# Kernel optimization log

Measured on AMD Instinct MI355X. Metric: run time of the kernel, lower is better.

## Reference

```python
import jax, jax.numpy as jnp
import numpy as np

B, N, C, H, R = 8, 1024, 768, 12, 64
HD = C // H


def setup_inputs() -> dict:
    key = jax.random.key(0)
    ks = jax.random.split(key, 16)
    def nrm(k, shape, s=0.02):
        return jax.random.normal(k, shape, jnp.float32) * s
    return {
        'x': jax.random.normal(ks[0], (B, N, C), jnp.float32),
        'Wqkv': nrm(ks[1], (3 * C, C)),
        'ssf_scale1': 1.0 + nrm(ks[2], (3 * C,)),
        'ssf_shift1': nrm(ks[3], (3 * C,)),
        'Wa': nrm(ks[4], (R, C)),            # LoRA down (sliced to sample_LoRA_dim)
        'Wb': nrm(ks[5], (3 * C, R)),        # LoRA up
        'Wrouter': nrm(ks[6], (2 * H * 3, C)),
        'brouter': nrm(ks[7], (2 * H * 3,)),
        'Wad_down': nrm(ks[8], (R, C)),      # parallel adapter down
        'bad_down': nrm(ks[9], (R,)),
        'Wad_up': nrm(ks[10], (3 * C, R)),   # parallel adapter up -> 3*dim
        'bad_up': nrm(ks[11], (3 * C,)),
        'Wproj': nrm(ks[12], (C, C)),
        'bproj': nrm(ks[13], (C,)),
        'ssf_scale2': 1.0 + nrm(ks[14], (C,)),
        'ssf_shift2': nrm(ks[15], (C,)),
    }


def reference(x, Wqkv, ssf_scale1, ssf_shift1, Wa, Wb, Wrouter, brouter,
              Wad_down, bad_down, Wad_up, bad_up, Wproj, bproj,
              ssf_scale2, ssf_shift2):
    Bx, Nx, Cx = x.shape
    scale = (Cx // H) ** -0.5

    def split_qkv(t):
        t = t.reshape(Bx, Nx, 3, H, Cx // H).transpose(2, 0, 3, 1, 4)
        return t[0], t[1], t[2]

    # base QKV with SSF scale-shift
    q, k, v = split_qkv((x @ Wqkv.T) * ssf_scale1 + ssf_shift1)
    # LoRA delta (dropout inactive at eval)
    ql, kl, vl = split_qkv((x @ Wa.T) @ Wb.T)
    # parallel adapter delta
    qp, kp, vp = split_qkv(jax.nn.gelu(x @ Wad_down.T + bad_down, approximate=False) @ Wad_up.T + bad_up)
    # router gating: sigmoid logits -> [B,N,3,H,2]
    rs = jax.nn.sigmoid(x @ Wrouter.T + brouter).reshape(Bx, Nx, 3, H, 2)
    # faithful to source: raw reshape [B,N,3,H] -> [B,N,H,3] (index-mixing), then transpose(1,2)
    rl = rs[..., 0].reshape(Bx, Nx, H, 3).transpose(0, 2, 1, 3)  # [B,H,N,3]
    rp = rs[..., 1].reshape(Bx, Nx, H, 3).transpose(0, 2, 1, 3)
    q = q + ql * rl[..., 0:1]
    k = k + kl * rl[..., 1:2] + kp * rp[..., 1:2]
    v = v + vl * rl[..., 2:3] + vp * rp[..., 2:3]
    # standard attention (prefix path disabled: prefix_dim=0)
    attn = jax.nn.softmax(jnp.einsum('bhnd,bhmd->bhnm', q, k) * scale, axis=-1)
    o = jnp.einsum('bhnm,bhmd->bhnd', attn, v).transpose(0, 2, 1, 3).reshape(Bx, Nx, Cx)
    return (o @ Wproj.T + bproj) * ssf_scale2 + ssf_shift2
```

## Files before the change

kernel.cpp:

```cpp
#include <hip/hip_runtime.h>
#include <math.h>

typedef unsigned short u16;
typedef unsigned int u32;
typedef short s16x8 __attribute__((ext_vector_type(8)));
typedef float f32x4 __attribute__((ext_vector_type(4)));
typedef float f32x16 __attribute__((ext_vector_type(16)));
typedef u16 u16x4 __attribute__((ext_vector_type(4)));

#define DEVI __device__ __forceinline__

DEVI u16 f2bf(float f) {
  unsigned u = __builtin_bit_cast(unsigned, f);
  u += 0x7fffu + ((u >> 16) & 1u);
  return (u16)(u >> 16);
}

DEVI u32 pack2bf(float a, float b) {
  return (u32)f2bf(a) | ((u32)f2bf(b) << 16);
}

DEVI f32x4 zero4() { f32x4 z; z[0]=0.f; z[1]=0.f; z[2]=0.f; z[3]=0.f; return z; }

DEVI float xor32_max(float x) { return fmaxf(x, __shfl_xor(x, 32, 64)); }
DEVI float xor32_sum(float x) { return x + __shfl_xor(x, 32, 64); }

#define MFMA16(a,b,c) __builtin_amdgcn_mfma_f32_16x16x32_bf16((a),(b),(c),0,0,0)
#define MFMA32(a,b,c) __builtin_amdgcn_mfma_f32_32x32x16_bf16((a),(b),(c),0,0,0)

#define GLD16(gp, lp) __builtin_amdgcn_global_load_lds( \
  (const __attribute__((address_space(1))) void*)(const void*)(gp), \
  (__attribute__((address_space(3))) void*)(void*)(lp), 16, 0, 0)


__global__ __launch_bounds__(256) void prep_x(const float* __restrict__ x,
                                              u16* __restrict__ Aaug) {
  const int i = blockIdx.x * 256 + threadIdx.x;
  if (i >= 8192 * 192) return;
  const int row = i / 192, c4 = (i - row * 192) * 4;
  const float4 v = *(const float4*)(x + (size_t)row * 768 + c4);
  u16x4 o; o[0]=f2bf(v.x); o[1]=f2bf(v.y); o[2]=f2bf(v.z); o[3]=f2bf(v.w);
  *(u16x4*)(Aaug + (size_t)row * 896 + c4) = o;
}

__global__ __launch_bounds__(256) void prep_w(
    const float* __restrict__ Wqkv, const float* __restrict__ s1,
    const float* __restrict__ Wb, const float* __restrict__ Wup,
    const float* __restrict__ Wa, const float* __restrict__ Wdn,
    const float* __restrict__ Wr, const float* __restrict__ Wp,
    u16* __restrict__ Baug, u16* __restrict__ Wsm, u16* __restrict__ Wpj) {
  const int i = blockIdx.x * 256 + threadIdx.x;
  const int N1 = 2304 * 896, N2 = N1 + 256 * 768, N3 = N2 + 768 * 768;
  if (i < N1) {
    const int c = i / 896, kk = i - c * 896;
    float v;
    if (kk < 768)      v = Wqkv[(size_t)c * 768 + kk] * s1[c];
    else if (kk < 832) v = Wb[(size_t)c * 64 + (kk - 768)];
    else               v = Wup[(size_t)c * 64 + (kk - 832)];
    Baug[i] = f2bf(v);
  } else if (i < N2) {
    const int j = i - N1; const int r = j / 768, kk = j - r * 768;
    float v = 0.0f;
    if (r < 64)       v = Wa[(size_t)r * 768 + kk];
    else if (r < 128) v = Wdn[(size_t)(r - 64) * 768 + kk];
    else if (r < 200) v = Wr[(size_t)(r - 128) * 768 + kk];
    Wsm[j] = f2bf(v);
  } else if (i < N3) {
    const int j = i - N2;
    Wpj[j] = f2bf(Wp[j]);
  }
}


template <int MODE>
__global__ __launch_bounds__(256)
void gemm_mfma(const u16* __restrict__ A, int lda,
               const u16* __restrict__ Bt, int ldb,
               const float* __restrict__ p0, const float* __restrict__ p1,
               const float* __restrict__ p2,
               u16* __restrict__ ob0, u16* __restrict__ ob1, u16* __restrict__ ob2,
               float* __restrict__ of0,
               const float* __restrict__ gates) {
  __shared__ __align__(16) u16 lds[2][8192];
  __shared__ float glds[2][2][128];
  const int tid = threadIdx.x;
  const int w = tid >> 6, l = tid & 63;
  const int rl = l & 15, gq = l >> 4;
  const int wrow = (w >> 1) * 64, wcol = (w & 1) * 64;
  const int br = blockIdx.x, bc = blockIdx.y;
  const int nt = (MODE == 2) ? 28 : 24;

  const int srow = l >> 2;
  const int sslot = (l & 3) ^ ((srow >> 1) & 3);
  const u16* aSrc = A + (size_t)(br * 128 + w * 32 + srow) * lda + sslot * 8;
  const u16* bSrc = Bt + (size_t)(bc * 128 + w * 32 + srow) * ldb + sslot * 8;

  int tq = 0;
  if constexpr (MODE == 2) {
    const int g = bc * 2 + (w & 1);
    tq = g / 12;
    {
      const int gsel = tid >> 7, rr = tid & 127;
      const int gg = bc * 2 + gsel;
      const int tt = gg / 12, hh = gg % 12;
      const int f = hh * 3 + tt;
      const int ridx = (f / 12) * 24 + (f % 12) * 2;
      glds[gsel][0][rr] = gates[(size_t)(br * 128 + rr) * 72 + ridx];
      glds[gsel][1][rr] = gates[(size_t)(br * 128 + rr) * 72 + ridx + 1];
    }
  }

  f32x4 acc[4][4];
#pragma unroll
  for (int i = 0; i < 4; ++i)
#pragma unroll
    for (int j = 0; j < 4; ++j) acc[i][j] = zero4();

  auto kt_of = [&](int t) {
    if constexpr (MODE == 2) return (t < 2) ? 26 + t : ((t < 4) ? 22 + t : t - 4);
    else return t;
  };
  auto stage = [&](int kt, int buf) {
    const size_t k0 = (size_t)kt * 32;
    GLD16(aSrc + k0, &lds[buf][(w * 32) * 32]);
    GLD16(aSrc + k0 + (size_t)16 * lda, &lds[buf][(w * 32 + 16) * 32]);
    GLD16(bSrc + k0, &lds[buf][4096 + (w * 32) * 32]);
    GLD16(bSrc + k0 + (size_t)16 * ldb, &lds[buf][4096 + (w * 32 + 16) * 32]);
  };

  stage(kt_of(0), 0);
  __syncthreads();

  for (int t = 0; t < nt; ++t) {
    const int buf = t & 1;
    if (t + 1 < nt) stage(kt_of(t + 1), buf ^ 1);
    const int sl = gq ^ ((rl >> 1) & 3);
    s16x8 af[4], bfv[4];
#pragma unroll
    for (int fr = 0; fr < 4; ++fr) {
      const int row = wrow + fr * 16 + rl;
      af[fr] = *(const s16x8*)&lds[buf][row * 32 + sl * 8];
    }
#pragma unroll
    for (int fc = 0; fc < 4; ++fc) {
      const int row = wcol + fc * 16 + rl;
      bfv[fc] = *(const s16x8*)&lds[buf][4096 + row * 32 + sl * 8];
    }
#pragma unroll
    for (int fr = 0; fr < 4; ++fr)
#pragma unroll
      for (int fc = 0; fc < 4; ++fc)
        acc[fr][fc] = MFMA16(af[fr], bfv[fc], acc[fr][fc]);

    if constexpr (MODE == 2) {
      if (t == 1 || t == 3) {
        const int wsel = w & 1;
        const bool ad = (t == 1);
#pragma unroll
        for (int fr = 0; fr < 4; ++fr)
#pragma unroll
          for (int r = 0; r < 4; ++r) {
            const int rloc = wrow + fr * 16 + gq * 4 + r;
            const float gl = glds[wsel][0][rloc];
            float s;
            if (ad) { const float gp = glds[wsel][1][rloc]; s = (tq > 0) ? gp / gl : 0.0f; }
            else s = gl;
#pragma unroll
            for (int fc = 0; fc < 4; ++fc) acc[fr][fc][r] *= s;
          }
      }
    }
    __syncthreads();
  }

  if constexpr (MODE == 0) {
#pragma unroll
    for (int fc = 0; fc < 4; ++fc) {
      const int col = bc * 128 + wcol + fc * 16 + rl;
#pragma unroll
      for (int fr = 0; fr < 4; ++fr)
#pragma unroll
        for (int r = 0; r < 4; ++r) {
          const int grow = br * 128 + wrow + fr * 16 + gq * 4 + r;
          const float v = acc[fr][fc][r];
          if (col < 64) {
            ob0[(size_t)grow * 896 + 768 + col] = f2bf(v);
          } else if (col < 128) {
            const float u = v + p0[col - 64];
            const float gv = 0.5f * u * (1.0f + erff(u * 0.70710678118654752f));
            ob0[(size_t)grow * 896 + 832 + (col - 64)] = f2bf(gv);
          } else if (col < 200) {
            const float z = v + p1[col - 128];
            of0[(size_t)grow * 72 + (col - 128)] = 1.0f / (1.0f + expf(-z));
          }
        }
    }
  } else if constexpr (MODE == 1) {
#pragma unroll
    for (int fc = 0; fc < 4; ++fc) {
      const int col = bc * 128 + wcol + fc * 16 + rl;
      const float bb = p0[col], sc = p1[col], sf = p2[col];
#pragma unroll
      for (int fr = 0; fr < 4; ++fr)
#pragma unroll
        for (int r = 0; r < 4; ++r) {
          const int grow = br * 128 + wrow + fr * 16 + gq * 4 + r;
          of0[(size_t)grow * 768 + col] = (acc[fr][fc][r] + bb) * sc + sf;
        }
    }
  } else {
    const int wsel = w & 1;
    const int bq = br >> 3;
    const int n0 = (br & 7) * 128;
    const int cbase = bc * 128 + wcol;
    const int hh = (cbase % 768) / 64;
    float s1v[4], buv[4];
#pragma unroll
    for (int fc = 0; fc < 4; ++fc) {
      const int col = cbase + fc * 16 + rl;
      s1v[fc] = p0[col];
      buv[fc] = (tq > 0) ? p1[col] : 0.0f;
    }
    if (tq < 2) {
      u16* dst = (tq == 0) ? ob0 : ob1;
      const float osc = (tq == 0) ? 0.125f : 1.0f;
#pragma unroll
      for (int fr = 0; fr < 4; ++fr)
#pragma unroll
        for (int r = 0; r < 4; ++r) {
          const int rloc = wrow + fr * 16 + gq * 4 + r;
          const float gp = glds[wsel][1][rloc];
          const int n = n0 + rloc;
#pragma unroll
          for (int fc = 0; fc < 4; ++fc) {
            const int d = fc * 16 + rl;
            const float v = (acc[fr][fc][r] + s1v[fc] + gp * buv[fc]) * osc;
            dst[((size_t)(bq * 12 + hh) * 1024 + n) * 64 + d] = f2bf(v);
          }
        }
    } else {
      u16* L = (u16*)&lds[0][0] + (size_t)w * 4096;
#pragma unroll
      for (int fr = 0; fr < 4; ++fr)
#pragma unroll
        for (int r = 0; r < 4; ++r) {
          const int rloc = wrow + fr * 16 + gq * 4 + r;
          const float gp = glds[wsel][1][rloc];
          const int nloc = fr * 16 + gq * 4 + r;
#pragma unroll
          for (int fc = 0; fc < 4; ++fc) {
            const int d = fc * 16 + rl;
            const float v = acc[fr][fc][r] + s1v[fc] + gp * buv[fc];
            L[(d * 64 + nloc) ^ ((d & 7) << 3)] = f2bf(v);
          }
        }
      const int nw = n0 + wrow;
#pragma unroll
      for (int it = 0; it < 8; ++it) {
        const int d = it * 8 + (l >> 3);
        const int slot = l & 7;
        const s16x8 val = *(const s16x8*)&L[d * 64 + ((slot ^ (d & 7)) << 3)];
        *(s16x8*)(ob2 + ((size_t)(bq * 12 + hh) * 64 + d) * 1024 + nw + slot * 8) = val;
      }
    }
  }
}


__global__ __launch_bounds__(256)
void attn2_kernel(const u16* __restrict__ Q, const u16* __restrict__ K,
                  const u16* __restrict__ VT, u16* __restrict__ AO) {
  __shared__ __align__(16) u16 kv[2][8192];
  const int tid = threadIdx.x, w = tid >> 6, l = tid & 63;
  const int l31 = l & 31, hi = l >> 5;
  const int bh = blockIdx.x % 96, qt = blockIdx.x / 96;
  const size_t kb = (size_t)bh * (1024 * 64);
  const float LOG2E = 1.4426950408889634f;
  const float THR = 5.545177f;

  const int q0 = qt * 128 + w * 32;
  s16x8 qf[4];
  {
    const u16* qp = Q + kb + (size_t)(q0 + l31) * 64 + hi * 8;
#pragma unroll
    for (int ks = 0; ks < 4; ++ks) qf[ks] = *(const s16x8*)(qp + ks * 16);
  }

  const int srow = l >> 3;
  const int sslot = (l & 7) ^ srow;
  const u16* kSrc = K + kb + (size_t)(w * 16 + srow) * 64 + sslot * 8;
  const u16* vSrc = VT + kb + (size_t)(w * 16 + srow) * 1024 + sslot * 8;
  auto stage = [&](int t, int buf) {
    const int kv0 = t * 64;
    GLD16(kSrc + (size_t)kv0 * 64, &kv[buf][(w * 16) * 64]);
    GLD16(kSrc + (size_t)kv0 * 64 + 8 * 64, &kv[buf][(w * 16 + 8) * 64]);
    GLD16(vSrc + kv0, &kv[buf][4096 + (w * 16) * 64]);
    GLD16(vSrc + kv0 + 8 * 1024, &kv[buf][4096 + (w * 16 + 8) * 64]);
  };

  f32x16 o0, o1;
#pragma unroll
  for (int r = 0; r < 16; ++r) { o0[r] = 0.f; o1[r] = 0.f; }
  float m = -1.0e30f, lsum = 0.f;

  const int swz = l31 & 7;

  stage(0, 0);
  __syncthreads();

  for (int t = 0; t < 16; ++t) {
    const int buf = t & 1;
    if (t < 15) stage(t + 1, buf ^ 1);

    f32x16 sA, sB;
#pragma unroll
    for (int r = 0; r < 16; ++r) { sA[r] = 0.f; sB[r] = 0.f; }
#pragma unroll
    for (int ks = 0; ks < 4; ++ks) {
      const int slot = (ks * 2 + hi) ^ swz;
      const s16x8 k0 = *(const s16x8*)&kv[buf][l31 * 64 + slot * 8];
      const s16x8 k1 = *(const s16x8*)&kv[buf][(32 + l31) * 64 + slot * 8];
      sA = MFMA32(k0, qf[ks], sA);
      sB = MFMA32(k1, qf[ks], sB);
    }

    float pm = sA[0];
#pragma unroll
    for (int r = 1; r < 16; ++r) pm = fmaxf(pm, sA[r]);
#pragma unroll
    for (int r = 0; r < 16; ++r) pm = fmaxf(pm, sB[r]);
    pm = xor32_max(pm);

    const bool need = pm > m + THR;
    if (__any(need)) {
      const float mnew = need ? pm : m;
      const float corr = __builtin_amdgcn_exp2f((m - mnew) * LOG2E);
      m = mnew;
      lsum *= corr;
#pragma unroll
      for (int r = 0; r < 16; ++r) {
        const int qrow = (r & 3) + 8 * (r >> 2) + 4 * hi;
        const float cr = __shfl(corr, qrow, 64);
        o0[r] *= cr; o1[r] *= cr;
      }
    }

    const float mL = m * LOG2E;
    float ps = 0.f;
#pragma unroll
    for (int r = 0; r < 16; ++r) {
      const float p = __builtin_amdgcn_exp2f(__builtin_fmaf(sA[r], LOG2E, -mL));
      sA[r] = p; ps += p;
    }
#pragma unroll
    for (int r = 0; r < 16; ++r) {
      const float p = __builtin_amdgcn_exp2f(__builtin_fmaf(sB[r], LOG2E, -mL));
      sB[r] = p; ps += p;
    }
    lsum += xor32_sum(ps);

    s16x8 pf[4];
#pragma unroll
    for (int s = 0; s < 4; ++s) {
      const f32x16 P = (s < 2) ? sA : sB;
      const int b = 8 * (s & 1);
      const u32 A0 = pack2bf(P[b + 0], P[b + 1]);
      const u32 A1 = pack2bf(P[b + 2], P[b + 3]);
      const u32 A2 = pack2bf(P[b + 4], P[b + 5]);
      const u32 A3 = pack2bf(P[b + 6], P[b + 7]);
      const u32 B0 = (u32)__shfl_xor((int)A0, 32, 64);
      const u32 B1 = (u32)__shfl_xor((int)A1, 32, 64);
      const u32 B2 = (u32)__shfl_xor((int)A2, 32, 64);
      const u32 B3 = (u32)__shfl_xor((int)A3, 32, 64);
      union { u32 u[4]; s16x8 v; } pk;
      pk.u[0] = hi ? B2 : A0;
      pk.u[1] = hi ? B3 : A1;
      pk.u[2] = hi ? A2 : B0;
      pk.u[3] = hi ? A3 : B1;
      pf[s] = pk.v;
    }

#pragma unroll
    for (int s = 0; s < 4; ++s) {
      const int slot = (s * 2 + hi) ^ swz;
      const s16x8 v0 = *(const s16x8*)&kv[buf][4096 + l31 * 64 + slot * 8];
      const s16x8 v1 = *(const s16x8*)&kv[buf][4096 + (32 + l31) * 64 + slot * 8];
      o0 = MFMA32(pf[s], v0, o0);
      o1 = MFMA32(pf[s], v1, o1);
    }
    __syncthreads();
  }

  const float invl = 1.0f / lsum;
  const int bq = bh / 12, h = bh % 12;
#pragma unroll
  for (int r = 0; r < 16; ++r) {
    const int qrow = (r & 3) + 8 * (r >> 2) + 4 * hi;
    const float ir = __shfl(invl, qrow, 64);
    const int n = q0 + qrow;
    u16* dst = AO + ((size_t)bq * 1024 + n) * 768 + h * 64 + l31;
    dst[0]  = f2bf(o0[r] * ir);
    dst[32] = f2bf(o1[r] * ir);
  }
}


extern "C" void kernel_launch(void* const* d_in, const int* in_sizes, int n_in,
                              void* d_out, int out_size, void* d_ws, size_t ws_size,
                              hipStream_t stream) {
  (void)in_sizes; (void)n_in; (void)out_size; (void)ws_size;
  const float* x    = (const float*)d_in[0];
  const float* Wqkv = (const float*)d_in[1];
  const float* s1   = (const float*)d_in[2];
  const float* sh1  = (const float*)d_in[3];
  const float* Wa   = (const float*)d_in[4];
  const float* Wb   = (const float*)d_in[5];
  const float* Wr   = (const float*)d_in[6];
  const float* brt  = (const float*)d_in[7];
  const float* Wdn  = (const float*)d_in[8];
  const float* bdn  = (const float*)d_in[9];
  const float* Wup  = (const float*)d_in[10];
  const float* bup  = (const float*)d_in[11];
  const float* Wp   = (const float*)d_in[12];
  const float* bpj  = (const float*)d_in[13];
  const float* sc2  = (const float*)d_in[14];
  const float* sf2  = (const float*)d_in[15];
  float* out = (float*)d_out;

  char* ws = (char*)d_ws;
  size_t off = 0;
  auto take = [&](size_t bytes) -> void* {
    void* p = ws + off;
    off = (off + bytes + 255) & ~(size_t)255;
    return p;
  };
  u16* Aaug = (u16*)take(8192UL * 896 * 2);
  u16* Baug = (u16*)take(2304UL * 896 * 2);
  u16* Wsm  = (u16*)take(256UL * 768 * 2);
  u16* Wpj  = (u16*)take(768UL * 768 * 2);
  float* gates = (float*)take(8192UL * 72 * 4);
  u16* qb  = (u16*)take(96UL * 1024 * 64 * 2);
  u16* kbf = (u16*)take(96UL * 1024 * 64 * 2);
  u16* vtb = (u16*)take(96UL * 64 * 1024 * 2);
  u16* ao  = (u16*)take(8192UL * 768 * 2);

  prep_x<<<dim3(6144), dim3(256), 0, stream>>>(x, Aaug);
  prep_w<<<dim3(11136), dim3(256), 0, stream>>>(Wqkv, s1, Wb, Wup, Wa, Wdn, Wr, Wp,
                                                Baug, Wsm, Wpj);
  gemm_mfma<0><<<dim3(64, 2), dim3(256), 0, stream>>>(
      Aaug, 896, Wsm, 768, bdn, brt, nullptr, Aaug, nullptr, nullptr, gates, nullptr);
  gemm_mfma<2><<<dim3(64, 18), dim3(256), 0, stream>>>(
      Aaug, 896, Baug, 896, sh1, bup, nullptr, qb, kbf, vtb, nullptr, gates);
  attn2_kernel<<<dim3(768), dim3(256), 0, stream>>>(qb, kbf, vtb, ao);
  gemm_mfma<1><<<dim3(64, 6), dim3(256), 0, stream>>>(
      ao, 768, Wpj, 768, bpj, sc2, sf2, nullptr, nullptr, nullptr, out, nullptr);
}
```

Before: 207.5 us.

## Stage Q/K epilogue through LDS, use manual vmcnt waits, cheaper P bf16 pack

In the QKV GEMM epilogue, the Q and K outputs are now written to a swizzled LDS tile and then stored with 16-byte vector writes, replacing scattered 2-byte global stores. The attention loop replaces __syncthreads with explicit s_waitcnt vmcnt plus s_barrier, so the prefetch of the next K/V tile can stay in flight while the current one is consumed. The probability pack switches from round-to-nearest-even to round-half-up using a byte permute, which trims ALU work but changes rounding slightly. The hand-placed waitcnt relies on exactly four outstanding loads per stage.

```diff
diff --git a/kernel.cpp b/kernel.cpp
--- a/kernel.cpp
+++ b/kernel.cpp
@@ -16,8 +16,10 @@
   return (u16)(u >> 16);
 }
 
-DEVI u32 pack2bf(float a, float b) {
-  return (u32)f2bf(a) | ((u32)f2bf(b) << 16);
+DEVI u32 pkbf_hu(float a, float b) {
+  const u32 ua = __builtin_bit_cast(u32, a) + 0x8000u;
+  const u32 ub = __builtin_bit_cast(u32, b) + 0x8000u;
+  return __builtin_amdgcn_perm(ub, ua, 0x07060302u);
 }
 
 DEVI f32x4 zero4() { f32x4 z; z[0]=0.f; z[1]=0.f; z[2]=0.f; z[3]=0.f; return z; }
@@ -222,22 +224,31 @@
       buv[fc] = (tq > 0) ? p1[col] : 0.0f;
     }
     if (tq < 2) {
+      u16* L = (u16*)&lds[0][0] + (size_t)w * 4096;
       u16* dst = (tq == 0) ? ob0 : ob1;
       const float osc = (tq == 0) ? 0.125f : 1.0f;
 #pragma unroll
       for (int fr = 0; fr < 4; ++fr)
 #pragma unroll
         for (int r = 0; r < 4; ++r) {
-          const int rloc = wrow + fr * 16 + gq * 4 + r;
-          const float gp = glds[wsel][1][rloc];
-          const int n = n0 + rloc;
+          const int nloc = fr * 16 + gq * 4 + r;
+          const float gp = glds[wsel][1][wrow + nloc];
 #pragma unroll
           for (int fc = 0; fc < 4; ++fc) {
             const int d = fc * 16 + rl;
             const float v = (acc[fr][fc][r] + s1v[fc] + gp * buv[fc]) * osc;
-            dst[((size_t)(bq * 12 + hh) * 1024 + n) * 64 + d] = f2bf(v);
+            L[nloc * 64 + (d ^ (gq << 4))] = f2bf(v);
           }
         }
+      const size_t rowbase = (size_t)(bq * 12 + hh) * 1024 + n0 + wrow;
+#pragma unroll
+      for (int it = 0; it < 8; ++it) {
+        const int nloc = it * 8 + (l >> 3);
+        const int sl8 = l & 7;
+        const s16x8 val =
+            *(const s16x8*)&L[nloc * 64 + ((sl8 * 8) ^ (((nloc >> 2) & 3) << 4))];
+        *(s16x8*)(dst + (rowbase + nloc) * 64 + sl8 * 8) = val;
+      }
     } else {
       u16* L = (u16*)&lds[0][0] + (size_t)w * 4096;
 #pragma unroll
@@ -306,11 +317,16 @@
   const int swz = l31 & 7;
 
   stage(0, 0);
-  __syncthreads();
 
   for (int t = 0; t < 16; ++t) {
     const int buf = t & 1;
-    if (t < 15) stage(t + 1, buf ^ 1);
+    if (t < 15) {
+      stage(t + 1, buf ^ 1);
+      asm volatile("s_waitcnt vmcnt(4)" ::: "memory");
+    } else {
+      asm volatile("s_waitcnt vmcnt(0)" ::: "memory");
+    }
+    __builtin_amdgcn_s_barrier();
 
     f32x16 sA, sB;
 #pragma unroll
@@ -364,10 +380,10 @@
     for (int s = 0; s < 4; ++s) {
       const f32x16 P = (s < 2) ? sA : sB;
       const int b = 8 * (s & 1);
-      const u32 A0 = pack2bf(P[b + 0], P[b + 1]);
-      const u32 A1 = pack2bf(P[b + 2], P[b + 3]);
-      const u32 A2 = pack2bf(P[b + 4], P[b + 5]);
-      const u32 A3 = pack2bf(P[b + 6], P[b + 7]);
+      const u32 A0 = pkbf_hu(P[b + 0], P[b + 1]);
+      const u32 A1 = pkbf_hu(P[b + 2], P[b + 3]);
+      const u32 A2 = pkbf_hu(P[b + 4], P[b + 5]);
+      const u32 A3 = pkbf_hu(P[b + 6], P[b + 7]);
       const u32 B0 = (u32)__shfl_xor((int)A0, 32, 64);
       const u32 B1 = (u32)__shfl_xor((int)A1, 32, 64);
       const u32 B2 = (u32)__shfl_xor((int)A2, 32, 64);
@@ -388,7 +404,7 @@
       o0 = MFMA32(pf[s], v0, o0);
       o1 = MFMA32(pf[s], v1, o1);
     }
-    __syncthreads();
+    __builtin_amdgcn_s_barrier();
   }
 
   const float invl = 1.0f / lsum;
```

Result: faster. 202.9 us (-2.2%).
